# Kernel optimization log

Hardware: AMD Instinct MI355X
Metric: run time of the kernel (lower is better)

Reference implementation:

```python
import jax, jax.numpy as jnp
import numpy as np

N_SEG, N_REG, N_EDGE, HID, CHEB_K = 40000, 1000, 640000, 256, 5


def setup_inputs() -> dict:
    key = jax.random.key(0)
    ks = jax.random.split(key, 6)
    return {
        "projected_region_features": jax.random.normal(ks[0], (N_REG, HID), jnp.float32),
        "segment2region_assignment": jax.random.uniform(ks[1], (N_SEG, N_REG), jnp.float32),
        "edge_index": jax.random.randint(ks[2], (2, N_EDGE), 0, N_SEG, dtype=jnp.int64),
        # ChebConv params: one [HID,HID] weight per Chebyshev order + shared bias
        "cheb_W": jax.random.normal(ks[3], (CHEB_K, HID, HID), jnp.float32) / np.sqrt(HID).astype(np.float32),
        "cheb_b": jnp.zeros((HID,), jnp.float32),
        "ln_gamma": jnp.ones((HID,), jnp.float32),
        "ln_beta": jnp.zeros((HID,), jnp.float32),
    }


def _cheb_conv(x, edge_index, W, b):
    """PyG ChebConv with normalization='sym', lambda_max=2.0.
    Scaled Laplacian L_hat = 2L/lam - I = -D^{-1/2} A D^{-1/2} (diag = 0)."""
    N = x.shape[0]
    src, dst = edge_index[0], edge_index[1]
    w = (src != dst).astype(x.dtype)  # remove_self_loops
    deg = jax.ops.segment_sum(w, src, num_segments=N)
    dinv = jnp.where(deg > 0, jax.lax.rsqrt(jnp.where(deg > 0, deg, 1.0)), 0.0)
    norm = -w * dinv[src] * dinv[dst]  # per-edge weight of L_hat

    def prop(t):  # y_i = sum_{(j->i)} norm_e * t_j
        return jax.ops.segment_sum(norm[:, None] * t[src], dst, num_segments=N)

    Tx0 = x
    out = Tx0 @ W[0]
    Tx1 = prop(Tx0)
    out = out + Tx1 @ W[1]
    for k in range(2, W.shape[0]):
        Tx2 = 2.0 * prop(Tx1) - Tx0
        out = out + Tx2 @ W[k]
        Tx0, Tx1 = Tx1, Tx2
    return out + b


def _layer_norm(x, g, b, eps=1e-5):
    mu = jnp.mean(x, axis=-1, keepdims=True)
    var = jnp.mean(jnp.square(x - mu), axis=-1, keepdims=True)
    return (x - mu) * jax.lax.rsqrt(var + eps) * g + b


def reference(projected_region_features, segment2region_assignment, edge_index,
              cheb_W, cheb_b, ln_gamma, ln_beta):
    # [n_seg, n_reg] @ [n_reg, hid] -> [n_seg, hid]
    seg_low_raw = segment2region_assignment @ projected_region_features
    seg_low = _cheb_conv(seg_low_raw, edge_index, cheb_W, cheb_b)
    seg_low = _layer_norm(jax.nn.gelu(seg_low, approximate=False), ln_gamma, ln_beta)
    return (seg_low, seg_low_raw)
```

## Files before the change

kernel.cpp:

```cpp
#include <hip/hip_runtime.h>

#define NSEG 40000
#define NREG 1000
#define NEDGE 640000
#define HID 256
#define KCAT 1280
#define KP1 1024
#define NBLK 157

typedef float f32x4 __attribute__((ext_vector_type(4)));
typedef short s16x8 __attribute__((ext_vector_type(8)));
typedef unsigned short u16x4 __attribute__((ext_vector_type(4)));
typedef unsigned short u16x8 __attribute__((ext_vector_type(8)));

typedef __attribute__((address_space(3))) unsigned int lds_u32;
typedef __attribute__((address_space(1))) const unsigned int glb_u32;

__device__ __forceinline__ void dma16(const void* g, void* l) {
    __builtin_amdgcn_global_load_lds((glb_u32*)g, (lds_u32*)l, 16, 0, 0);
}

__device__ __forceinline__ unsigned short f2bf(float f) {
    unsigned u = __builtin_bit_cast(unsigned, f);
    u += 0x7FFFu + ((u >> 16) & 1u);
    return (unsigned short)(u >> 16);
}
__device__ __forceinline__ float bf2f(unsigned short h) {
    unsigned u = ((unsigned)h) << 16;
    return __builtin_bit_cast(float, u);
}

__device__ __forceinline__ f32x4 mfma16(s16x8 a, s16x8 b, f32x4 c) {
    return __builtin_amdgcn_mfma_f32_16x16x32_bf16(a, b, c, 0, 0, 0);
}

__global__ void detect_kernel(const unsigned int* __restrict__ E, int* flag) {
    int lane = threadIdx.x;
    unsigned v = E[2 * lane + 1];
    unsigned long long m = __ballot(v == 0u);
    if (lane == 0) *flag = (__popcll(m) >= 48) ? 1 : 0;
}

__device__ __forceinline__ int edge_at(const void* E, int idx, int is64) {
    return is64 ? (int)((const long long*)E)[idx] : ((const int*)E)[idx];
}

__global__ __launch_bounds__(256) void deg_cnt_kernel(const void* __restrict__ E,
                                                      const int* __restrict__ flag,
                                                      int* deg, int* cnt) {
    int e = blockIdx.x * 256 + threadIdx.x;
    if (e >= NEDGE) return;
    int is64 = *flag;
    int s = edge_at(E, e, is64);
    int d = edge_at(E, e + NEDGE, is64);
    if (s != d) {
        atomicAdd(&deg[s], 1);
        atomicAdd(&cnt[d], 1);
    }
}

__global__ __launch_bounds__(256) void dinv_kernel(const int* __restrict__ deg,
                                                   float* __restrict__ dinv) {
    int i = blockIdx.x * 256 + threadIdx.x;
    if (i < NSEG) {
        int d = deg[i];
        dinv[i] = d > 0 ? rsqrtf((float)d) : 0.f;
    }
}

__global__ __launch_bounds__(256) void scan1_kernel(const int* __restrict__ cnt,
                                                    int* __restrict__ bsum) {
    __shared__ int sh[256];
    int t = threadIdx.x;
    int i = blockIdx.x * 256 + t;
    sh[t] = (i < NSEG) ? cnt[i] : 0;
    __syncthreads();
    for (int o = 128; o > 0; o >>= 1) {
        if (t < o) sh[t] += sh[t + o];
        __syncthreads();
    }
    if (t == 0) bsum[blockIdx.x] = sh[0];
}

__global__ __launch_bounds__(256) void scan2_kernel(const int* __restrict__ bsum,
                                                    int* __restrict__ boff,
                                                    int* __restrict__ rowptr) {
    __shared__ int sh[256];
    int t = threadIdx.x;
    int v = (t < NBLK) ? bsum[t] : 0;
    sh[t] = v;
    __syncthreads();
    for (int o = 1; o < 256; o <<= 1) {
        int x = 0;
        if (t >= o) x = sh[t - o];
        __syncthreads();
        if (t >= o) sh[t] += x;
        __syncthreads();
    }
    if (t < NBLK) boff[t] = sh[t] - v;
    if (t == 255) rowptr[NSEG] = sh[255];
}

__global__ __launch_bounds__(256) void scan3_kernel(const int* __restrict__ cnt,
                                                    const int* __restrict__ boff,
                                                    int* __restrict__ rowptr,
                                                    int* __restrict__ cursor) {
    __shared__ int sh[256];
    int t = threadIdx.x;
    int i = blockIdx.x * 256 + t;
    int v = (i < NSEG) ? cnt[i] : 0;
    sh[t] = v;
    __syncthreads();
    for (int o = 1; o < 256; o <<= 1) {
        int x = 0;
        if (t >= o) x = sh[t - o];
        __syncthreads();
        if (t >= o) sh[t] += x;
        __syncthreads();
    }
    if (i < NSEG) {
        int p = boff[blockIdx.x] + sh[t] - v;
        rowptr[i] = p;
        cursor[i] = p;
    }
}

__global__ __launch_bounds__(256) void scatter_kernel(const void* __restrict__ E,
                                                      const int* __restrict__ flag,
                                                      const float* __restrict__ dinv,
                                                      int* cursor,
                                                      int* __restrict__ colidx,
                                                      float* __restrict__ val) {
    int e = blockIdx.x * 256 + threadIdx.x;
    if (e >= NEDGE) return;
    int is64 = *flag;
    int s = edge_at(E, e, is64);
    int d = edge_at(E, e + NEDGE, is64);
    if (s != d) {
        int pos = atomicAdd(&cursor[d], 1);
        colidx[pos] = s;
        val[pos] = -dinv[s] * dinv[d];
    }
}

__global__ void prep_pt_kernel(const float* __restrict__ P, unsigned short* __restrict__ Pt) {
    int n = blockIdx.x;
    for (int k = threadIdx.x; k < KP1; k += blockDim.x)
        Pt[(size_t)n * KP1 + k] = (k < NREG) ? f2bf(P[(size_t)k * HID + n]) : (unsigned short)0;
}
__global__ void prep_wt_kernel(const float* __restrict__ W, unsigned short* __restrict__ Wt) {
    int n = blockIdx.x;
    for (int k = threadIdx.x; k < KCAT; k += blockDim.x)
        Wt[(size_t)n * KCAT + k] = f2bf(W[(size_t)k * HID + n]);
}

__global__ __launch_bounds__(512) void gemm1_kernel(const float* __restrict__ S,
                                                    const unsigned short* __restrict__ Pt,
                                                    float* __restrict__ raw,
                                                    unsigned short* __restrict__ xcat) {
    __shared__ unsigned short As[2][128 * 32];
    __shared__ unsigned short Bs[2][256 * 32];
    const int tid = threadIdx.x;
    const int lane = tid & 63, wid = tid >> 6;
    const int wm = wid >> 2, wn = wid & 3;
    const int r = lane & 15, q = lane >> 4;
    const int qx8 = (q ^ (r & 3)) << 3;
    const int m0 = blockIdx.x * 128;
    const int arow = tid >> 2, acol = (tid & 3) * 8;
    const int ag = ((acol >> 3) ^ (arow & 3)) << 3;
    const int j0 = 2 * wid, j1 = j0 + 1;
    const int brow0 = j0 * 16 + (lane >> 2), brow1 = j1 * 16 + (lane >> 2);
    const int bcol = (((lane & 3) ^ ((lane >> 2) & 3)) << 3);

    f32x4 acc[4][4] = {};
    const int srow_c = (m0 + arow < NSEG) ? (m0 + arow) : (NSEG - 1);
    const float* aptr = S + (size_t)srow_c * NREG;

    auto stageB = [&](int c, int kb) {
        dma16(Pt + (size_t)brow0 * KP1 + kb + bcol, &Bs[c][j0 * 512]);
        dma16(Pt + (size_t)brow1 * KP1 + kb + bcol, &Bs[c][j1 * 512]);
    };
    auto loadA = [&](int kb) -> f32x4* {
        static __shared__ char dummy;
        return nullptr;
    };
    (void)loadA;

    stageB(0, 0);
    {
        int k0 = 0 + acol;
        f32x4 f0 = *(const f32x4*)(aptr + k0);
        f32x4 f1 = *(const f32x4*)(aptr + k0 + 4);
        u16x8 o = {f2bf(f0[0]), f2bf(f0[1]), f2bf(f0[2]), f2bf(f0[3]),
                   f2bf(f1[0]), f2bf(f1[1]), f2bf(f1[2]), f2bf(f1[3])};
        *(u16x8*)&As[0][arow * 32 + ag] = o;
    }
    __syncthreads();

    for (int t = 0; t < 32; ++t) {
        const int c = t & 1;
        f32x4 f0, f1;
        if (t < 31) {
            stageB(c ^ 1, (t + 1) * 32);
            int k0 = (t + 1) * 32 + acol;
            if (k0 + 8 > NREG) k0 = 0;
            f0 = *(const f32x4*)(aptr + k0);
            f1 = *(const f32x4*)(aptr + k0 + 4);
        }
        s16x8 af[4], bfv[4];
#pragma unroll
        for (int am = 0; am < 4; ++am)
            af[am] = *(const s16x8*)&As[c][(wm * 64 + am * 16 + r) * 32 + qx8];
#pragma unroll
        for (int bn = 0; bn < 4; ++bn)
            bfv[bn] = *(const s16x8*)&Bs[c][(wn * 64 + bn * 16 + r) * 32 + qx8];
#pragma unroll
        for (int am = 0; am < 4; ++am)
#pragma unroll
            for (int bn = 0; bn < 4; ++bn)
                acc[am][bn] = mfma16(af[am], bfv[bn], acc[am][bn]);
        if (t < 31) {
            u16x8 o = {f2bf(f0[0]), f2bf(f0[1]), f2bf(f0[2]), f2bf(f0[3]),
                       f2bf(f1[0]), f2bf(f1[1]), f2bf(f1[2]), f2bf(f1[3])};
            *(u16x8*)&As[c ^ 1][arow * 32 + ag] = o;
        }
        __syncthreads();
    }

#pragma unroll
    for (int am = 0; am < 4; ++am) {
        int rowb = m0 + wm * 64 + am * 16 + q * 4;
#pragma unroll
        for (int bn = 0; bn < 4; ++bn) {
            int col = wn * 64 + bn * 16 + r;
#pragma unroll
            for (int i = 0; i < 4; ++i) {
                int row = rowb + i;
                if (row < NSEG) {
                    float v = acc[am][bn][i];
                    raw[(size_t)row * HID + col] = v;
                    xcat[(size_t)row * KCAT + col] = f2bf(v);
                }
            }
        }
    }
}

__global__ __launch_bounds__(256) void prop_kernel(unsigned short* xcat,
                                                   const int* __restrict__ rowptr,
                                                   const int* __restrict__ colidx,
                                                   const float* __restrict__ val,
                                                   int inOff, int outOff, int subOff,
                                                   float scale) {
    int g = blockIdx.x * 4 + (threadIdx.x >> 6);
    int lane = threadIdx.x & 63;
    int e0 = rowptr[g], e1 = rowptr[g + 1];
    float a0 = 0.f, a1 = 0.f, a2 = 0.f, a3 = 0.f;
    const unsigned short* xin = xcat + inOff + lane * 4;
    for (int base = e0; base < e1; base += 64) {
        int m = e1 - base;
        if (m > 64) m = 64;
        int cc = 0;
        float vv = 0.f;
        if (lane < m) {
            cc = colidx[base + lane];
            vv = val[base + lane];
        }
        int i = 0;
        for (; i + 8 <= m; i += 8) {
            u16x4 t[8];
#pragma unroll
            for (int j = 0; j < 8; ++j) {
                int c = __shfl(cc, i + j);
                t[j] = *(const u16x4*)(xin + (size_t)c * KCAT);
            }
#pragma unroll
            for (int j = 0; j < 8; ++j) {
                float v = __shfl(vv, i + j);
                a0 += v * bf2f(t[j][0]);
                a1 += v * bf2f(t[j][1]);
                a2 += v * bf2f(t[j][2]);
                a3 += v * bf2f(t[j][3]);
            }
        }
        for (; i < m; ++i) {
            int c = __shfl(cc, i);
            float v = __shfl(vv, i);
            u16x4 t = *(const u16x4*)(xin + (size_t)c * KCAT);
            a0 += v * bf2f(t[0]);
            a1 += v * bf2f(t[1]);
            a2 += v * bf2f(t[2]);
            a3 += v * bf2f(t[3]);
        }
    }
    a0 *= scale; a1 *= scale; a2 *= scale; a3 *= scale;
    if (subOff >= 0) {
        u16x4 p = *(const u16x4*)(xcat + (size_t)g * KCAT + subOff + lane * 4);
        a0 -= bf2f(p[0]); a1 -= bf2f(p[1]); a2 -= bf2f(p[2]); a3 -= bf2f(p[3]);
    }
    u16x4 o = {f2bf(a0), f2bf(a1), f2bf(a2), f2bf(a3)};
    *(u16x4*)(xcat + (size_t)g * KCAT + outOff + lane * 4) = o;
}

__global__ __launch_bounds__(512) void gemm2_kernel(const unsigned short* __restrict__ xcat,
                                                    const unsigned short* __restrict__ Wt,
                                                    const float* __restrict__ bias,
                                                    const float* __restrict__ gamma,
                                                    const float* __restrict__ beta,
                                                    float* __restrict__ outp) {
    __shared__ unsigned short As[2][128 * 32];
    __shared__ unsigned short Bs[2][256 * 32];
    __shared__ float rs[128][4];
    __shared__ float rss[128][4];
    const int tid = threadIdx.x;
    const int lane = tid & 63, wid = tid >> 6;
    const int wm = wid >> 2, wn = wid & 3;
    const int r = lane & 15, q = lane >> 4;
    const int qx8 = (q ^ (r & 3)) << 3;
    const int m0 = blockIdx.x * 128;
    const int crow = lane >> 2;
    const int bcol = (((lane & 3) ^ ((lane >> 2) & 3)) << 3);

    f32x4 acc[4][4] = {};

    auto stage = [&](int c, int kb) {
#pragma unroll
        for (int k = 0; k < 3; ++k) {
            int idx = 3 * wid + k;
            if (idx < 16) {
                int n = idx * 16 + crow;
                dma16(Wt + (size_t)n * KCAT + kb + bcol, &Bs[c][idx * 512]);
            } else {
                int a = idx - 16;
                int row = m0 + a * 16 + crow;
                dma16(xcat + (size_t)row * KCAT + kb + bcol, &As[c][a * 512]);
            }
        }
    };

    stage(0, 0);
    __syncthreads();

    for (int t = 0; t < 40; ++t) {
        const int c = t & 1;
        if (t < 39) stage(c ^ 1, (t + 1) * 32);
        s16x8 af[4], bfv[4];
#pragma unroll
        for (int am = 0; am < 4; ++am)
            af[am] = *(const s16x8*)&As[c][(wm * 64 + am * 16 + r) * 32 + qx8];
#pragma unroll
        for (int bn = 0; bn < 4; ++bn)
            bfv[bn] = *(const s16x8*)&Bs[c][(wn * 64 + bn * 16 + r) * 32 + qx8];
#pragma unroll
        for (int am = 0; am < 4; ++am)
#pragma unroll
            for (int bn = 0; bn < 4; ++bn)
                acc[am][bn] = mfma16(af[am], bfv[bn], acc[am][bn]);
        __syncthreads();
    }

    float bc[4], gm[4], bt[4];
#pragma unroll
    for (int bn = 0; bn < 4; ++bn) {
        int col = wn * 64 + bn * 16 + r;
        bc[bn] = bias[col];
        gm[bn] = gamma[col];
        bt[bn] = beta[col];
    }
#pragma unroll
    for (int am = 0; am < 4; ++am) {
#pragma unroll
        for (int i = 0; i < 4; ++i) {
            float s = 0.f, ss = 0.f;
#pragma unroll
            for (int bn = 0; bn < 4; ++bn) {
                float v = acc[am][bn][i] + bc[bn];
                v = 0.5f * v * (1.f + erff(v * 0.70710678118654752f));
                acc[am][bn][i] = v;
                s += v;
                ss += v * v;
            }
#pragma unroll
            for (int msk = 1; msk < 16; msk <<= 1) {
                s += __shfl_xor(s, msk);
                ss += __shfl_xor(ss, msk);
            }
            if (r == 0) {
                int row = wm * 64 + am * 16 + q * 4 + i;
                rs[row][wn] = s;
                rss[row][wn] = ss;
            }
        }
    }
    __syncthreads();
#pragma unroll
    for (int am = 0; am < 4; ++am) {
#pragma unroll
        for (int i = 0; i < 4; ++i) {
            int row = wm * 64 + am * 16 + q * 4 + i;
            float s = rs[row][0] + rs[row][1] + rs[row][2] + rs[row][3];
            float ss = rss[row][0] + rss[row][1] + rss[row][2] + rss[row][3];
            float mu = s * (1.f / HID);
            float var = ss * (1.f / HID) - mu * mu;
            float inv = rsqrtf(var + 1e-5f);
            if (m0 + row < NSEG) {
#pragma unroll
                for (int bn = 0; bn < 4; ++bn) {
                    int col = wn * 64 + bn * 16 + r;
                    outp[(size_t)(m0 + row) * HID + col] = (acc[am][bn][i] - mu) * inv * gm[bn] + bt[bn];
                }
            }
        }
    }
}

extern "C" void kernel_launch(void* const* d_in, const int* in_sizes, int n_in,
                              void* d_out, int out_size, void* d_ws, size_t ws_size,
                              hipStream_t stream) {
    const float* P     = (const float*)d_in[0];
    const float* S     = (const float*)d_in[1];
    const void*  E     = d_in[2];
    const float* W     = (const float*)d_in[3];
    const float* bias  = (const float*)d_in[4];
    const float* gamma = (const float*)d_in[5];
    const float* beta  = (const float*)d_in[6];

    float* out = (float*)d_out;
    float* raw = out + (size_t)NSEG * HID;

    char* ws = (char*)d_ws;
    size_t off = 0;
    auto alloc = [&](size_t bytes) -> void* {
        void* p = ws + off;
        off += (bytes + 255) & ~(size_t)255;
        return p;
    };
    unsigned short* xcat   = (unsigned short*)alloc((size_t)NSEG * KCAT * 2);
    unsigned short* Pt     = (unsigned short*)alloc((size_t)HID * KP1 * 2);
    unsigned short* Wt     = (unsigned short*)alloc((size_t)HID * KCAT * 2);
    int*            deg    = (int*)alloc((size_t)NSEG * 4);
    float*          dinv   = (float*)alloc((size_t)NSEG * 4);
    int*            cnt    = (int*)alloc((size_t)NSEG * 4);
    int*            rowptr = (int*)alloc((size_t)(NSEG + 1) * 4);
    int*            cursor = (int*)alloc((size_t)NSEG * 4);
    int*            colidx = (int*)alloc((size_t)NEDGE * 4);
    float*          val    = (float*)alloc((size_t)NEDGE * 4);
    int*            bsum   = (int*)alloc((size_t)NBLK * 4);
    int*            boff   = (int*)alloc((size_t)NBLK * 4);
    int*            flag   = (int*)alloc(256);
    if (off > ws_size) return;

    hipMemsetAsync(deg, 0, (size_t)NSEG * 4, stream);
    hipMemsetAsync(cnt, 0, (size_t)NSEG * 4, stream);

    detect_kernel<<<1, 64, 0, stream>>>((const unsigned int*)E, flag);
    prep_pt_kernel<<<HID, 256, 0, stream>>>(P, Pt);
    prep_wt_kernel<<<HID, 256, 0, stream>>>(W, Wt);

    deg_cnt_kernel<<<NEDGE / 256, 256, 0, stream>>>(E, flag, deg, cnt);
    dinv_kernel<<<(NSEG + 255) / 256, 256, 0, stream>>>(deg, dinv);
    scan1_kernel<<<NBLK, 256, 0, stream>>>(cnt, bsum);
    scan2_kernel<<<1, 256, 0, stream>>>(bsum, boff, rowptr);
    scan3_kernel<<<NBLK, 256, 0, stream>>>(cnt, boff, rowptr, cursor);
    scatter_kernel<<<NEDGE / 256, 256, 0, stream>>>(E, flag, dinv, cursor, colidx, val);

    gemm1_kernel<<<(NSEG + 127) / 128, 512, 0, stream>>>(S, Pt, raw, xcat);

    prop_kernel<<<NSEG / 4, 256, 0, stream>>>(xcat, rowptr, colidx, val, 0 * HID, 1 * HID, -1, 1.f);
    prop_kernel<<<NSEG / 4, 256, 0, stream>>>(xcat, rowptr, colidx, val, 1 * HID, 2 * HID, 0 * HID, 2.f);
    prop_kernel<<<NSEG / 4, 256, 0, stream>>>(xcat, rowptr, colidx, val, 2 * HID, 3 * HID, 1 * HID, 2.f);
    prop_kernel<<<NSEG / 4, 256, 0, stream>>>(xcat, rowptr, colidx, val, 3 * HID, 4 * HID, 2 * HID, 2.f);

    gemm2_kernel<<<(NSEG + 127) / 128, 512, 0, stream>>>(xcat, Wt, bias, gamma, beta, out);
}
```

Measured before the change: 445.2 us.

## Simplify gemm1 to 64-row tiles with single-buffered padded LDS

Rewrites the first GEMM to use 64-row blocks of 256 threads instead of 128-row blocks of 512 threads. The async global-to-LDS DMA and double buffering are replaced by plain register loads into a single padded shared-memory tile, which also removes the XOR swizzle. The aim is more resident blocks, higher occupancy and simpler addressing. In exchange, loads no longer overlap with MFMA compute, and the projection matrix is re-read by twice as many blocks, which raises L2 traffic.

New measurement: 436.8 us. About the same (-1.9%).

```diff
diff --git a/kernel.cpp b/kernel.cpp
--- a/kernel.cpp
+++ b/kernel.cpp
@@ -6,6 +6,7 @@
 #define HID 256
 #define KCAT 1280
 #define KP1 1024
+#define LPAD 40
 #define NBLK 157
 
 typedef float f32x4 __attribute__((ext_vector_type(4)));
@@ -154,93 +155,65 @@
         Wt[(size_t)n * KCAT + k] = f2bf(W[(size_t)k * HID + n]);
 }
 
-__global__ __launch_bounds__(512) void gemm1_kernel(const float* __restrict__ S,
+__global__ __launch_bounds__(256) void gemm1_kernel(const float* __restrict__ S,
                                                     const unsigned short* __restrict__ Pt,
                                                     float* __restrict__ raw,
                                                     unsigned short* __restrict__ xcat) {
-    __shared__ unsigned short As[2][128 * 32];
-    __shared__ unsigned short Bs[2][256 * 32];
+    __shared__ unsigned short As[64][LPAD];
+    __shared__ unsigned short Bs[256][LPAD];
+    const int m0 = blockIdx.x * 64;
     const int tid = threadIdx.x;
-    const int lane = tid & 63, wid = tid >> 6;
-    const int wm = wid >> 2, wn = wid & 3;
+    const int lane = tid & 63, wn = tid >> 6;
     const int r = lane & 15, q = lane >> 4;
-    const int qx8 = (q ^ (r & 3)) << 3;
-    const int m0 = blockIdx.x * 128;
-    const int arow = tid >> 2, acol = (tid & 3) * 8;
-    const int ag = ((acol >> 3) ^ (arow & 3)) << 3;
-    const int j0 = 2 * wid, j1 = j0 + 1;
-    const int brow0 = j0 * 16 + (lane >> 2), brow1 = j1 * 16 + (lane >> 2);
-    const int bcol = (((lane & 3) ^ ((lane >> 2) & 3)) << 3);
+    const int srow = tid >> 2, scol = (tid & 3) * 8;
 
     f32x4 acc[4][4] = {};
-    const int srow_c = (m0 + arow < NSEG) ? (m0 + arow) : (NSEG - 1);
-    const float* aptr = S + (size_t)srow_c * NREG;
-
-    auto stageB = [&](int c, int kb) {
-        dma16(Pt + (size_t)brow0 * KP1 + kb + bcol, &Bs[c][j0 * 512]);
-        dma16(Pt + (size_t)brow1 * KP1 + kb + bcol, &Bs[c][j1 * 512]);
-    };
-    auto loadA = [&](int kb) -> f32x4* {
-        static __shared__ char dummy;
-        return nullptr;
-    };
-    (void)loadA;
-
-    stageB(0, 0);
-    {
-        int k0 = 0 + acol;
-        f32x4 f0 = *(const f32x4*)(aptr + k0);
-        f32x4 f1 = *(const f32x4*)(aptr + k0 + 4);
-        u16x8 o = {f2bf(f0[0]), f2bf(f0[1]), f2bf(f0[2]), f2bf(f0[3]),
-                   f2bf(f1[0]), f2bf(f1[1]), f2bf(f1[2]), f2bf(f1[3])};
-        *(u16x8*)&As[0][arow * 32 + ag] = o;
-    }
-    __syncthreads();
-
-    for (int t = 0; t < 32; ++t) {
-        const int c = t & 1;
-        f32x4 f0, f1;
-        if (t < 31) {
-            stageB(c ^ 1, (t + 1) * 32);
-            int k0 = (t + 1) * 32 + acol;
-            if (k0 + 8 > NREG) k0 = 0;
-            f0 = *(const f32x4*)(aptr + k0);
-            f1 = *(const f32x4*)(aptr + k0 + 4);
-        }
+
+    for (int kb = 0; kb < NREG; kb += 32) {
+        const bool kvalid = (kb + scol + 8 <= NREG);
+        u16x8 av = {0, 0, 0, 0, 0, 0, 0, 0};
+        u16x8 bv0 = av, bv1 = av, bv2 = av, bv3 = av;
+        if (kvalid) {
+            const float* sp = S + (size_t)(m0 + srow) * NREG + kb + scol;
+            f32x4 f0 = *(const f32x4*)sp;
+            f32x4 f1 = *(const f32x4*)(sp + 4);
+            av[0] = f2bf(f0[0]); av[1] = f2bf(f0[1]); av[2] = f2bf(f0[2]); av[3] = f2bf(f0[3]);
+            av[4] = f2bf(f1[0]); av[5] = f2bf(f1[1]); av[6] = f2bf(f1[2]); av[7] = f2bf(f1[3]);
+            bv0 = *(const u16x8*)(Pt + (size_t)(srow)       * KP1 + kb + scol);
+            bv1 = *(const u16x8*)(Pt + (size_t)(srow +  64) * KP1 + kb + scol);
+            bv2 = *(const u16x8*)(Pt + (size_t)(srow + 128) * KP1 + kb + scol);
+            bv3 = *(const u16x8*)(Pt + (size_t)(srow + 192) * KP1 + kb + scol);
+        }
+        __syncthreads();
+        *(u16x8*)&As[srow][scol] = av;
+        *(u16x8*)&Bs[srow][scol] = bv0;
+        *(u16x8*)&Bs[srow + 64][scol] = bv1;
+        *(u16x8*)&Bs[srow + 128][scol] = bv2;
+        *(u16x8*)&Bs[srow + 192][scol] = bv3;
+        __syncthreads();
         s16x8 af[4], bfv[4];
 #pragma unroll
-        for (int am = 0; am < 4; ++am)
-            af[am] = *(const s16x8*)&As[c][(wm * 64 + am * 16 + r) * 32 + qx8];
-#pragma unroll
-        for (int bn = 0; bn < 4; ++bn)
-            bfv[bn] = *(const s16x8*)&Bs[c][(wn * 64 + bn * 16 + r) * 32 + qx8];
-#pragma unroll
-        for (int am = 0; am < 4; ++am)
+        for (int am = 0; am < 4; ++am) af[am] = *(const s16x8*)&As[am * 16 + r][q * 8];
+#pragma unroll
+        for (int bn = 0; bn < 4; ++bn) bfv[bn] = *(const s16x8*)&Bs[wn * 64 + bn * 16 + r][q * 8];
+#pragma unroll
+        for (int am = 0; am < 4; ++am) {
 #pragma unroll
             for (int bn = 0; bn < 4; ++bn)
                 acc[am][bn] = mfma16(af[am], bfv[bn], acc[am][bn]);
-        if (t < 31) {
-            u16x8 o = {f2bf(f0[0]), f2bf(f0[1]), f2bf(f0[2]), f2bf(f0[3]),
-                       f2bf(f1[0]), f2bf(f1[1]), f2bf(f1[2]), f2bf(f1[3])};
-            *(u16x8*)&As[c ^ 1][arow * 32 + ag] = o;
-        }
-        __syncthreads();
-    }
-
+        }
+    }
 #pragma unroll
     for (int am = 0; am < 4; ++am) {
-        int rowb = m0 + wm * 64 + am * 16 + q * 4;
+        int rowb = m0 + am * 16 + q * 4;
 #pragma unroll
         for (int bn = 0; bn < 4; ++bn) {
             int col = wn * 64 + bn * 16 + r;
 #pragma unroll
             for (int i = 0; i < 4; ++i) {
-                int row = rowb + i;
-                if (row < NSEG) {
-                    float v = acc[am][bn][i];
-                    raw[(size_t)row * HID + col] = v;
-                    xcat[(size_t)row * KCAT + col] = f2bf(v);
-                }
+                float v = acc[am][bn][i];
+                raw[(size_t)(rowb + i) * HID + col] = v;
+                xcat[(size_t)(rowb + i) * KCAT + col] = f2bf(v);
             }
         }
     }
@@ -464,7 +437,7 @@
     scan3_kernel<<<NBLK, 256, 0, stream>>>(cnt, boff, rowptr, cursor);
     scatter_kernel<<<NEDGE / 256, 256, 0, stream>>>(E, flag, dinv, cursor, colidx, val);
 
-    gemm1_kernel<<<(NSEG + 127) / 128, 512, 0, stream>>>(S, Pt, raw, xcat);
+    gemm1_kernel<<<NSEG / 64, 256, 0, stream>>>(S, Pt, raw, xcat);
 
     prop_kernel<<<NSEG / 4, 256, 0, stream>>>(xcat, rowptr, colidx, val, 0 * HID, 1 * HID, -1, 1.f);
     prop_kernel<<<NSEG / 4, 256, 0, stream>>>(xcat, rowptr, colidx, val, 1 * HID, 2 * HID, 0 * HID, 2.f);
```
